# Kernel optimization log

Hardware: AMD Instinct MI355X
Metric: run time of the kernel (lower is better)

The kernel has to match this reference:

```python
import jax, jax.numpy as jnp
import numpy as np

N = 50000
E = 800000
D = 128
H = 8
DH = D // H


def setup_inputs() -> dict:
    key = jax.random.key(0)
    ks = jax.random.split(key, 8)
    x = jax.random.normal(ks[0], (N, D), dtype=jnp.float32)
    src = jax.random.randint(ks[1], (E,), 0, N, dtype=jnp.int32)
    dst = jax.random.randint(ks[2], (E,), 0, N, dtype=jnp.int32)
    s = 1.0 / np.sqrt(D)
    w_qkv = jax.random.uniform(ks[3], (3 * D, D), jnp.float32, -s, s)
    b_qkv = jax.random.uniform(ks[4], (3 * D,), jnp.float32, -s, s)
    w_out = jax.random.uniform(ks[5], (D, D), jnp.float32, -s, s)
    b_out = jax.random.uniform(ks[6], (D,), jnp.float32, -s, s)
    return {"x": x, "src": src, "dst": dst, "w_qkv": w_qkv, "b_qkv": b_qkv,
            "w_out": w_out, "b_out": b_out}


def reference(x, src, dst, w_qkv, b_qkv, w_out, b_out):
    n = x.shape[0]
    coef = 1.0 / np.sqrt(DH)
    qkv = (x @ w_qkv.T + b_qkv).reshape(n, H, 3 * DH)
    q, k, v = qkv[..., :DH], qkv[..., DH:2 * DH], qkv[..., 2 * DH:]
    # per-edge scores: dot(k[src], q[dst]) per head -> [E, H]
    scores = jnp.einsum('ehd,ehd->eh', k[src], q[dst]) * coef
    # edge softmax over edges sharing the same destination node
    smax = jax.ops.segment_max(scores, dst, num_segments=n)  # [N, H]
    smax = jnp.where(jnp.isfinite(smax), smax, 0.0)
    ex = jnp.exp(scores - smax[dst])                          # [E, H]
    denom = jax.ops.segment_sum(ex, dst, num_segments=n)      # [N, H]
    probs = ex / jnp.maximum(denom[dst], 1e-30)
    # weighted aggregation of source values -> [N, H, DH]
    agg = jax.ops.segment_sum(probs[:, :, None] * v[src], dst, num_segments=n)
    out = agg.reshape(n, D) @ w_out.T + b_out
    return out
```

## Files before the change

kernel.cpp:

```cpp
#include <hip/hip_runtime.h>
#include <math.h>

#define DD   128
#define NQKV 384
#define CAP  128

typedef __attribute__((ext_vector_type(8))) short          bf16x8;
typedef __attribute__((ext_vector_type(8))) unsigned short ushort8;
typedef __attribute__((ext_vector_type(4))) float          f32x4;

__device__ __forceinline__ unsigned short f2bf(float f) {
    unsigned u = __float_as_uint(f);
    u += 0x7fffu + ((u >> 16) & 1u);
    return (unsigned short)(u >> 16);
}
__device__ __forceinline__ float bf2f(unsigned short h) {
    return __uint_as_float(((unsigned)h) << 16);
}
__device__ __forceinline__ float bflo(unsigned u) { return __uint_as_float(u << 16); }
__device__ __forceinline__ float bfhi(unsigned u) { return __uint_as_float(u & 0xffff0000u); }

#define NWQ8 (NQKV * DD / 8)
#define NWO8 (DD * DD / 8)

__global__ void prep_kernel(const float* __restrict__ w_qkv, const float* __restrict__ w_out,
                            unsigned short* __restrict__ wq_hi, unsigned short* __restrict__ wq_lo,
                            unsigned short* __restrict__ wo_hi, unsigned short* __restrict__ wo_lo,
                            int* __restrict__ counts, int nzc4) {
    int i = blockIdx.x * blockDim.x + threadIdx.x;
    if (i < nzc4) {
        ((int4*)counts)[i] = make_int4(0, 0, 0, 0);
        return;
    }
    int j = i - nzc4;
    const float* srcp;
    unsigned short *hip_, *lop_;
    if (j < NWQ8)            { srcp = w_qkv + (size_t)j * 8;          hip_ = wq_hi + (size_t)j * 8;          lop_ = wq_lo + (size_t)j * 8; }
    else if (j < NWQ8+NWO8)  { int k = j - NWQ8; srcp = w_out + (size_t)k * 8; hip_ = wo_hi + (size_t)k * 8; lop_ = wo_lo + (size_t)k * 8; }
    else return;
    const float4* p = (const float4*)srcp;
    float4 a = p[0], b = p[1];
    float v[8] = {a.x, a.y, a.z, a.w, b.x, b.y, b.z, b.w};
    ushort8 vh, vl;
    #pragma unroll
    for (int t = 0; t < 8; ++t) {
        unsigned short h = f2bf(v[t]);
        vh[t] = h;
        vl[t] = f2bf(v[t] - bf2f(h));
    }
    *(ushort8*)hip_ = vh;
    *(ushort8*)lop_ = vl;
}

__global__ void scatter_fixed_kernel(const int* __restrict__ src, const int* __restrict__ dst,
                                     int* __restrict__ counts, int* __restrict__ lists, int E) {
    int t = blockIdx.x * blockDim.x + threadIdx.x;
    int base = t * 8;
    if (base >= E) return;
    if (base + 8 <= E) {
        int4 d0 = *(const int4*)(dst + base);
        int4 d1 = *(const int4*)(dst + base + 4);
        int4 s0 = *(const int4*)(src + base);
        int4 s1 = *(const int4*)(src + base + 4);
        int dd[8] = {d0.x, d0.y, d0.z, d0.w, d1.x, d1.y, d1.z, d1.w};
        int ss[8] = {s0.x, s0.y, s0.z, s0.w, s1.x, s1.y, s1.z, s1.w};
        int pos[8];
        #pragma unroll
        for (int i = 0; i < 8; ++i) pos[i] = atomicAdd(&counts[dd[i]], 1);
        #pragma unroll
        for (int i = 0; i < 8; ++i)
            if (pos[i] < CAP) lists[(size_t)dd[i] * CAP + pos[i]] = ss[i];
    } else {
        for (int e = base; e < E; ++e) {
            int d = dst[e];
            int pos = atomicAdd(&counts[d], 1);
            if (pos < CAP) lists[(size_t)d * CAP + pos] = src[e];
        }
    }
}

#define TM 128
#define TN 128
#define LDA 40

__global__ __launch_bounds__(256, 3) void qkv_gemm_kernel(
    const float* __restrict__ X,
    const unsigned short* __restrict__ Bh, const unsigned short* __restrict__ Bl,
    const float* __restrict__ bias, unsigned short* __restrict__ Cq,
    unsigned short* __restrict__ Ck, unsigned short* __restrict__ Cv, int M)
{
    __shared__ unsigned short As[TM * LDA];
    __shared__ unsigned short Bs_h[TN * LDA];
    __shared__ unsigned short Bs_l[TN * LDA];

    const int tid  = threadIdx.x;
    const int l    = tid & 63;
    const int wv   = tid >> 6;
    const int quad = l >> 4;
    const int l15  = l & 15;
    const int wm   = (wv & 1) * 64;
    const int wn   = (wv >> 1) * 64;
    const int n0   = blockIdx.x * TN;
    const int m0   = blockIdx.y * TM;

    f32x4 acc[4][4];
    #pragma unroll
    for (int i = 0; i < 4; ++i)
        #pragma unroll
        for (int j = 0; j < 4; ++j) acc[i][j] = (f32x4)0.f;

    #pragma unroll
    for (int kc = 0; kc < DD; kc += 32) {
        #pragma unroll
        for (int it = 0; it < 2; ++it) {
            int idx = tid + it * 256;
            int row = idx >> 2;
            int pc  = idx & 3;
            int loff = row * LDA + pc * 8;
            ushort8 va = 0;
            if (m0 + row < M) {
                const float4* xp = (const float4*)(X + (size_t)(m0 + row) * DD + kc + pc * 8);
                float4 a0 = xp[0], a1 = xp[1];
                float v[8] = {a0.x,a0.y,a0.z,a0.w,a1.x,a1.y,a1.z,a1.w};
                #pragma unroll
                for (int t = 0; t < 8; ++t) va[t] = f2bf(v[t]);
            }
            *(ushort8*)&As[loff] = va;
            size_t gb = (size_t)(n0 + row) * DD + kc + pc * 8;
            *(ushort8*)&Bs_h[loff] = *(const ushort8*)(Bh + gb);
            *(ushort8*)&Bs_l[loff] = *(const ushort8*)(Bl + gb);
        }
        __syncthreads();

        bf16x8 ah[4], bh[4], bl[4];
        #pragma unroll
        for (int mt = 0; mt < 4; ++mt)
            ah[mt] = *(const bf16x8*)&As[(wm + mt * 16 + l15) * LDA + quad * 8];
        #pragma unroll
        for (int nt = 0; nt < 4; ++nt) {
            int off = (wn + nt * 16 + l15) * LDA + quad * 8;
            bh[nt] = *(const bf16x8*)&Bs_h[off];
            bl[nt] = *(const bf16x8*)&Bs_l[off];
        }
        #pragma unroll
        for (int mt = 0; mt < 4; ++mt)
            #pragma unroll
            for (int nt = 0; nt < 4; ++nt) {
                acc[mt][nt] = __builtin_amdgcn_mfma_f32_16x16x32_bf16(ah[mt], bh[nt], acc[mt][nt], 0, 0, 0);
                acc[mt][nt] = __builtin_amdgcn_mfma_f32_16x16x32_bf16(ah[mt], bl[nt], acc[mt][nt], 0, 0, 0);
            }
        __syncthreads();
    }

    #pragma unroll
    for (int nt = 0; nt < 4; ++nt) {
        int j = n0 + wn + nt * 16 + l15;
        float bj = bias[j];
        int h = j / 48;
        int r = j - h * 48;
        int seg = (r >= 32) ? 2 : ((r >= 16) ? 1 : 0);
        int bc  = h * 16 + r - seg * 16;
        unsigned short* dstp = (seg == 0 ? Cq : (seg == 1 ? Ck : Cv));
        #pragma unroll
        for (int mt = 0; mt < 4; ++mt)
            #pragma unroll
            for (int rr = 0; rr < 4; ++rr) {
                int m = m0 + wm + mt * 16 + quad * 4 + rr;
                if (m < M) dstp[(size_t)m * DD + bc] = f2bf(acc[mt][nt][rr] + bj);
            }
    }
}

__global__ __launch_bounds__(256, 3) void out_gemm_kernel(
    const unsigned short* __restrict__ A,
    const unsigned short* __restrict__ Bh, const unsigned short* __restrict__ Bl,
    const float* __restrict__ bias, float* __restrict__ C, int M)
{
    __shared__ unsigned short As[TM * LDA];
    __shared__ unsigned short Bs_h[TN * LDA];
    __shared__ unsigned short Bs_l[TN * LDA];

    const int tid  = threadIdx.x;
    const int l    = tid & 63;
    const int wv   = tid >> 6;
    const int quad = l >> 4;
    const int l15  = l & 15;
    const int wm   = (wv & 1) * 64;
    const int wn   = (wv >> 1) * 64;
    const int m0   = blockIdx.x * TM;

    f32x4 acc[4][4];
    #pragma unroll
    for (int i = 0; i < 4; ++i)
        #pragma unroll
        for (int j = 0; j < 4; ++j) acc[i][j] = (f32x4)0.f;

    #pragma unroll
    for (int kc = 0; kc < DD; kc += 32) {
        #pragma unroll
        for (int it = 0; it < 2; ++it) {
            int idx = tid + it * 256;
            int row = idx >> 2;
            int pc  = idx & 3;
            int loff = row * LDA + pc * 8;
            ushort8 va = 0;
            if (m0 + row < M)
                va = *(const ushort8*)(A + (size_t)(m0 + row) * DD + kc + pc * 8);
            *(ushort8*)&As[loff] = va;
            size_t gb = (size_t)row * DD + kc + pc * 8;
            *(ushort8*)&Bs_h[loff] = *(const ushort8*)(Bh + gb);
            *(ushort8*)&Bs_l[loff] = *(const ushort8*)(Bl + gb);
        }
        __syncthreads();

        bf16x8 ah[4], bh[4], bl[4];
        #pragma unroll
        for (int mt = 0; mt < 4; ++mt)
            ah[mt] = *(const bf16x8*)&As[(wm + mt * 16 + l15) * LDA + quad * 8];
        #pragma unroll
        for (int nt = 0; nt < 4; ++nt) {
            int off = (wn + nt * 16 + l15) * LDA + quad * 8;
            bh[nt] = *(const bf16x8*)&Bs_h[off];
            bl[nt] = *(const bf16x8*)&Bs_l[off];
        }
        #pragma unroll
        for (int mt = 0; mt < 4; ++mt)
            #pragma unroll
            for (int nt = 0; nt < 4; ++nt) {
                acc[mt][nt] = __builtin_amdgcn_mfma_f32_16x16x32_bf16(ah[mt], bh[nt], acc[mt][nt], 0, 0, 0);
                acc[mt][nt] = __builtin_amdgcn_mfma_f32_16x16x32_bf16(ah[mt], bl[nt], acc[mt][nt], 0, 0, 0);
            }
        __syncthreads();
    }

    #pragma unroll
    for (int nt = 0; nt < 4; ++nt) {
        int j = wn + nt * 16 + l15;
        float bj = bias[j];
        #pragma unroll
        for (int mt = 0; mt < 4; ++mt)
            #pragma unroll
            for (int rr = 0; rr < 4; ++rr) {
                int m = m0 + wm + mt * 16 + quad * 4 + rr;
                if (m < M) C[(size_t)m * DD + j] = acc[mt][nt][rr] + bj;
            }
    }
}

__global__ __launch_bounds__(256) void wave_attn_kernel(
    const unsigned short* __restrict__ qbf, const unsigned short* __restrict__ kbf,
    const unsigned short* __restrict__ vbf, const int* __restrict__ lists,
    const int* __restrict__ counts,
    unsigned short* __restrict__ agg, int N)
{
    const int lane = threadIdx.x & 63;
    const int n = blockIdx.x * 4 + (threadIdx.x >> 6);
    if (n >= N) return;

    const int h = lane >> 3;
    const int e = lane & 7;

    const int deg = min(counts[n], CAP);
    const size_t obase = (size_t)n * DD + 2 * lane;
    if (deg == 0) {
        *(unsigned*)(agg + obase) = 0u;
        return;
    }

    const int row0 = n * CAP;

    const uint4* qp = (const uint4*)(qbf + (size_t)n * DD + h * 16);
    const uint4 qa = qp[0], qb = qp[1];
    const float4 q0 = make_float4(bflo(qa.x), bfhi(qa.x), bflo(qa.y), bfhi(qa.y));
    const float4 q1 = make_float4(bflo(qa.z), bfhi(qa.z), bflo(qa.w), bfhi(qa.w));
    const float4 q2 = make_float4(bflo(qb.x), bfhi(qb.x), bflo(qb.y), bfhi(qb.y));
    const float4 q3 = make_float4(bflo(qb.z), bfhi(qb.z), bflo(qb.w), bfhi(qb.w));

    int cur = lists[row0 + min(e, deg - 1)];
    int nxt = lists[row0 + min(8 + e, deg - 1)];

    const uint4* kp0 = (const uint4*)(kbf + (size_t)cur * DD + h * 16);
    uint4 ka = kp0[0], kb = kp0[1];
    unsigned vv[8];
    #pragma unroll
    for (int ee = 0; ee < 8; ++ee)
        vv[ee] = *(const unsigned*)(vbf + (size_t)__shfl(cur, ee) * DD + 2 * lane);

    float l_run = 0.f;
    float acc0 = 0.f, acc1 = 0.f;

    for (int c = 0; c < deg; c += 8) {
        const int cnt = min(8, deg - c);
        const bool more = (c + 8 < deg);

        const int nn = lists[row0 + min(c + 16 + e, deg - 1)];

        uint4 k1a = ka, k1b = kb;
        unsigned vn[8];
        #pragma unroll
        for (int ee = 0; ee < 8; ++ee) vn[ee] = vv[ee];
        if (more) {
            const uint4* kp = (const uint4*)(kbf + (size_t)nxt * DD + h * 16);
            k1a = kp[0]; k1b = kp[1];
            #pragma unroll
            for (int ee = 0; ee < 8; ++ee)
                vn[ee] = *(const unsigned*)(vbf + (size_t)__shfl(nxt, ee) * DD + 2 * lane);
        }

        float s = bflo(ka.x)*q0.x + bfhi(ka.x)*q0.y + bflo(ka.y)*q0.z + bfhi(ka.y)*q0.w
                + bflo(ka.z)*q1.x + bfhi(ka.z)*q1.y + bflo(ka.w)*q1.z + bfhi(ka.w)*q1.w
                + bflo(kb.x)*q2.x + bfhi(kb.x)*q2.y + bflo(kb.y)*q2.z + bfhi(kb.y)*q2.w
                + bflo(kb.z)*q3.x + bfhi(kb.z)*q3.y + bflo(kb.w)*q3.z + bfhi(kb.w)*q3.w;

        const float p = (e < cnt) ? __expf(s * 0.25f) : 0.f;
        l_run += p;

        #pragma unroll
        for (int ee = 0; ee < 8; ++ee) {
            const float pe = __shfl(p, (lane & 0x38) | ee);
            acc0 = fmaf(pe, bflo(vv[ee]), acc0);
            acc1 = fmaf(pe, bfhi(vv[ee]), acc1);
        }

        ka = k1a; kb = k1b;
        #pragma unroll
        for (int ee = 0; ee < 8; ++ee) vv[ee] = vn[ee];
        cur = nxt; nxt = nn;
    }

    l_run += __shfl_xor(l_run, 1);
    l_run += __shfl_xor(l_run, 2);
    l_run += __shfl_xor(l_run, 4);

    const float inv = 1.f / fmaxf(l_run, 1e-30f);
    const float o0 = acc0 * inv, o1 = acc1 * inv;
    *(unsigned*)(agg + obase) = (unsigned)f2bf(o0) | ((unsigned)f2bf(o1) << 16);
}

extern "C" void kernel_launch(void* const* d_in, const int* in_sizes, int n_in,
                              void* d_out, int out_size, void* d_ws, size_t ws_size,
                              hipStream_t stream) {
    const float* x     = (const float*)d_in[0];
    const int*   src   = (const int*)  d_in[1];
    const int*   dst   = (const int*)  d_in[2];
    const float* w_qkv = (const float*)d_in[3];
    const float* b_qkv = (const float*)d_in[4];
    const float* w_out = (const float*)d_in[5];
    const float* b_out = (const float*)d_in[6];
    float* out = (float*)d_out;

    const int N = in_sizes[0] / DD;
    const int E = in_sizes[1];

    typedef unsigned short u16;
    char* ws = (char*)d_ws;
    u16* qbf   = (u16*)ws;   ws += (size_t)N * DD * sizeof(u16);
    u16* kbf   = (u16*)ws;   ws += (size_t)N * DD * sizeof(u16);
    u16* vbf   = (u16*)ws;   ws += (size_t)N * DD * sizeof(u16);
    u16* aggb  = (u16*)ws;   ws += (size_t)N * DD * sizeof(u16);
    u16* wq_hi = (u16*)ws;   ws += (size_t)NQKV * DD * sizeof(u16);
    u16* wq_lo = (u16*)ws;   ws += (size_t)NQKV * DD * sizeof(u16);
    u16* wo_hi = (u16*)ws;   ws += (size_t)DD * DD * sizeof(u16);
    u16* wo_lo = (u16*)ws;   ws += (size_t)DD * DD * sizeof(u16);
    int* counts = (int*)ws;  ws += (size_t)((N + 3) / 4 * 4) * sizeof(int);
    int* lists  = (int*)ws;  ws += (size_t)N * CAP * sizeof(int);

    const int nzc4 = (N + 3) / 4;
    const int npb  = (nzc4 + NWQ8 + NWO8 + 255) / 256;
    const int nsb  = ((E + 7) / 8 + 255) / 256;
    const int MB   = (N + TM - 1) / TM;

    prep_kernel<<<npb, 256, 0, stream>>>(w_qkv, w_out, wq_hi, wq_lo, wo_hi, wo_lo,
                                         counts, nzc4);
    scatter_fixed_kernel<<<nsb, 256, 0, stream>>>(src, dst, counts, lists, E);

    qkv_gemm_kernel<<<dim3(NQKV / TN, MB), 256, 0, stream>>>(
        x, wq_hi, wq_lo, b_qkv, qbf, kbf, vbf, N);

    wave_attn_kernel<<<(N + 3) / 4, 256, 0, stream>>>(
        qbf, kbf, vbf, lists, counts, aggb, N);

    out_gemm_kernel<<<MB, 256, 0, stream>>>(
        aggb, wo_hi, wo_lo, b_out, out, N);
}
```

Baseline: 235.4 us.

## Stage full-K A tile once in LDS and read weights directly from global

```diff
diff --git a/kernel.cpp b/kernel.cpp
--- a/kernel.cpp
+++ b/kernel.cpp
@@ -81,17 +81,15 @@
 
 #define TM 128
 #define TN 128
-#define LDA 40
-
-__global__ __launch_bounds__(256, 3) void qkv_gemm_kernel(
+#define LDK 136
+
+__global__ __launch_bounds__(256, 2) void qkv_gemm_kernel(
     const float* __restrict__ X,
     const unsigned short* __restrict__ Bh, const unsigned short* __restrict__ Bl,
     const float* __restrict__ bias, unsigned short* __restrict__ Cq,
     unsigned short* __restrict__ Ck, unsigned short* __restrict__ Cv, int M)
 {
-    __shared__ unsigned short As[TM * LDA];
-    __shared__ unsigned short Bs_h[TN * LDA];
-    __shared__ unsigned short Bs_l[TN * LDA];
+    __shared__ unsigned short As[TM * LDK];
 
     const int tid  = threadIdx.x;
     const int l    = tid & 63;
@@ -100,8 +98,25 @@
     const int l15  = l & 15;
     const int wm   = (wv & 1) * 64;
     const int wn   = (wv >> 1) * 64;
-    const int n0   = blockIdx.x * TN;
-    const int m0   = blockIdx.y * TM;
+    const int m0   = blockIdx.x * TM;
+    const int n0   = blockIdx.y * TN;
+
+    #pragma unroll
+    for (int it = 0; it < 8; ++it) {
+        int idx = tid + it * 256;
+        int row = idx >> 4;
+        int pc  = idx & 15;
+        ushort8 va = 0;
+        if (m0 + row < M) {
+            const float4* xp = (const float4*)(X + (size_t)(m0 + row) * DD + pc * 8);
+            float4 a0 = xp[0], a1 = xp[1];
+            float v[8] = {a0.x,a0.y,a0.z,a0.w,a1.x,a1.y,a1.z,a1.w};
+            #pragma unroll
+            for (int t = 0; t < 8; ++t) va[t] = f2bf(v[t]);
+        }
+        *(ushort8*)&As[row * LDK + pc * 8] = va;
+    }
+    __syncthreads();
 
     f32x4 acc[4][4];
     #pragma unroll
@@ -110,38 +125,18 @@
         for (int j = 0; j < 4; ++j) acc[i][j] = (f32x4)0.f;
 
     #pragma unroll
-    for (int kc = 0; kc < DD; kc += 32) {
-        #pragma unroll
-        for (int it = 0; it < 2; ++it) {
-            int idx = tid + it * 256;
-            int row = idx >> 2;
-            int pc  = idx & 3;
-            int loff = row * LDA + pc * 8;
-            ushort8 va = 0;
-            if (m0 + row < M) {
-                const float4* xp = (const float4*)(X + (size_t)(m0 + row) * DD + kc + pc * 8);
-                float4 a0 = xp[0], a1 = xp[1];
-                float v[8] = {a0.x,a0.y,a0.z,a0.w,a1.x,a1.y,a1.z,a1.w};
-                #pragma unroll
-                for (int t = 0; t < 8; ++t) va[t] = f2bf(v[t]);
-            }
-            *(ushort8*)&As[loff] = va;
-            size_t gb = (size_t)(n0 + row) * DD + kc + pc * 8;
-            *(ushort8*)&Bs_h[loff] = *(const ushort8*)(Bh + gb);
-            *(ushort8*)&Bs_l[loff] = *(const ushort8*)(Bl + gb);
-        }
-        __syncthreads();
-
+    for (int kk = 0; kk < 4; ++kk) {
+        const int ko = kk * 32 + quad * 8;
         bf16x8 ah[4], bh[4], bl[4];
         #pragma unroll
-        for (int mt = 0; mt < 4; ++mt)
-            ah[mt] = *(const bf16x8*)&As[(wm + mt * 16 + l15) * LDA + quad * 8];
-        #pragma unroll
         for (int nt = 0; nt < 4; ++nt) {
-            int off = (wn + nt * 16 + l15) * LDA + quad * 8;
-            bh[nt] = *(const bf16x8*)&Bs_h[off];
-            bl[nt] = *(const bf16x8*)&Bs_l[off];
-        }
+            size_t gb = (size_t)(n0 + wn + nt * 16 + l15) * DD + ko;
+            bh[nt] = *(const bf16x8*)(Bh + gb);
+            bl[nt] = *(const bf16x8*)(Bl + gb);
+        }
+        #pragma unroll
+        for (int mt = 0; mt < 4; ++mt)
+            ah[mt] = *(const bf16x8*)&As[(wm + mt * 16 + l15) * LDK + ko];
         #pragma unroll
         for (int mt = 0; mt < 4; ++mt)
             #pragma unroll
@@ -149,7 +144,6 @@
                 acc[mt][nt] = __builtin_amdgcn_mfma_f32_16x16x32_bf16(ah[mt], bh[nt], acc[mt][nt], 0, 0, 0);
                 acc[mt][nt] = __builtin_amdgcn_mfma_f32_16x16x32_bf16(ah[mt], bl[nt], acc[mt][nt], 0, 0, 0);
             }
-        __syncthreads();
     }
 
     #pragma unroll
@@ -171,14 +165,12 @@
     }
 }
 
-__global__ __launch_bounds__(256, 3) void out_gemm_kernel(
+__global__ __launch_bounds__(256, 2) void out_gemm_kernel(
     const unsigned short* __restrict__ A,
     const unsigned short* __restrict__ Bh, const unsigned short* __restrict__ Bl,
     const float* __restrict__ bias, float* __restrict__ C, int M)
 {
-    __shared__ unsigned short As[TM * LDA];
-    __shared__ unsigned short Bs_h[TN * LDA];
-    __shared__ unsigned short Bs_l[TN * LDA];
+    __shared__ unsigned short As[TM * LDK];
 
     const int tid  = threadIdx.x;
     const int l    = tid & 63;
@@ -189,6 +181,18 @@
     const int wn   = (wv >> 1) * 64;
     const int m0   = blockIdx.x * TM;
 
+    #pragma unroll
+    for (int it = 0; it < 8; ++it) {
+        int idx = tid + it * 256;
+        int row = idx >> 4;
+        int pc  = idx & 15;
+        ushort8 va = 0;
+        if (m0 + row < M)
+            va = *(const ushort8*)(A + (size_t)(m0 + row) * DD + pc * 8);
+        *(ushort8*)&As[row * LDK + pc * 8] = va;
+    }
+    __syncthreads();
+
     f32x4 acc[4][4];
     #pragma unroll
     for (int i = 0; i < 4; ++i)
@@ -196,33 +200,18 @@
         for (int j = 0; j < 4; ++j) acc[i][j] = (f32x4)0.f;
 
     #pragma unroll
-    for (int kc = 0; kc < DD; kc += 32) {
-        #pragma unroll
-        for (int it = 0; it < 2; ++it) {
-            int idx = tid + it * 256;
-            int row = idx >> 2;
-            int pc  = idx & 3;
-            int loff = row * LDA + pc * 8;
-            ushort8 va = 0;
-            if (m0 + row < M)
-                va = *(const ushort8*)(A + (size_t)(m0 + row) * DD + kc + pc * 8);
-            *(ushort8*)&As[loff] = va;
-            size_t gb = (size_t)row * DD + kc + pc * 8;
-            *(ushort8*)&Bs_h[loff] = *(const ushort8*)(Bh + gb);
-            *(ushort8*)&Bs_l[loff] = *(const ushort8*)(Bl + gb);
-        }
-        __syncthreads();
-
+    for (int kk = 0; kk < 4; ++kk) {
+        const int ko = kk * 32 + quad * 8;
         bf16x8 ah[4], bh[4], bl[4];
         #pragma unroll
-        for (int mt = 0; mt < 4; ++mt)
-            ah[mt] = *(const bf16x8*)&As[(wm + mt * 16 + l15) * LDA + quad * 8];
-        #pragma unroll
         for (int nt = 0; nt < 4; ++nt) {
-            int off = (wn + nt * 16 + l15) * LDA + quad * 8;
-            bh[nt] = *(const bf16x8*)&Bs_h[off];
-            bl[nt] = *(const bf16x8*)&Bs_l[off];
-        }
+            size_t gb = (size_t)(wn + nt * 16 + l15) * DD + ko;
+            bh[nt] = *(const bf16x8*)(Bh + gb);
+            bl[nt] = *(const bf16x8*)(Bl + gb);
+        }
+        #pragma unroll
+        for (int mt = 0; mt < 4; ++mt)
+            ah[mt] = *(const bf16x8*)&As[(wm + mt * 16 + l15) * LDK + ko];
         #pragma unroll
         for (int mt = 0; mt < 4; ++mt)
             #pragma unroll
@@ -230,7 +219,6 @@
                 acc[mt][nt] = __builtin_amdgcn_mfma_f32_16x16x32_bf16(ah[mt], bh[nt], acc[mt][nt], 0, 0, 0);
                 acc[mt][nt] = __builtin_amdgcn_mfma_f32_16x16x32_bf16(ah[mt], bl[nt], acc[mt][nt], 0, 0, 0);
             }
-        __syncthreads();
     }
 
     #pragma unroll
@@ -374,7 +362,7 @@
                                          counts, nzc4);
     scatter_fixed_kernel<<<nsb, 256, 0, stream>>>(src, dst, counts, lists, E);
 
-    qkv_gemm_kernel<<<dim3(NQKV / TN, MB), 256, 0, stream>>>(
+    qkv_gemm_kernel<<<dim3(MB, NQKV / TN), 256, 0, stream>>>(
         x, wq_hi, wq_lo, b_qkv, qbf, kbf, vbf, N);
 
     wave_attn_kernel<<<(N + 3) / 4, 256, 0, stream>>>(
```

Result: slower. 252.1 us (+7.1%).

## Fuse weight bf16 split into GEMMs, memset counts, packed-float attention math

Applied to the files above, without the earlier changes.

```diff
diff --git a/kernel.cpp b/kernel.cpp
--- a/kernel.cpp
+++ b/kernel.cpp
@@ -8,6 +8,7 @@
 typedef __attribute__((ext_vector_type(8))) short          bf16x8;
 typedef __attribute__((ext_vector_type(8))) unsigned short ushort8;
 typedef __attribute__((ext_vector_type(4))) float          f32x4;
+typedef __attribute__((ext_vector_type(2))) float          f32x2;
 
 __device__ __forceinline__ unsigned short f2bf(float f) {
     unsigned u = __float_as_uint(f);
@@ -19,37 +20,8 @@
 }
 __device__ __forceinline__ float bflo(unsigned u) { return __uint_as_float(u << 16); }
 __device__ __forceinline__ float bfhi(unsigned u) { return __uint_as_float(u & 0xffff0000u); }
-
-#define NWQ8 (NQKV * DD / 8)
-#define NWO8 (DD * DD / 8)
-
-__global__ void prep_kernel(const float* __restrict__ w_qkv, const float* __restrict__ w_out,
-                            unsigned short* __restrict__ wq_hi, unsigned short* __restrict__ wq_lo,
-                            unsigned short* __restrict__ wo_hi, unsigned short* __restrict__ wo_lo,
-                            int* __restrict__ counts, int nzc4) {
-    int i = blockIdx.x * blockDim.x + threadIdx.x;
-    if (i < nzc4) {
-        ((int4*)counts)[i] = make_int4(0, 0, 0, 0);
-        return;
-    }
-    int j = i - nzc4;
-    const float* srcp;
-    unsigned short *hip_, *lop_;
-    if (j < NWQ8)            { srcp = w_qkv + (size_t)j * 8;          hip_ = wq_hi + (size_t)j * 8;          lop_ = wq_lo + (size_t)j * 8; }
-    else if (j < NWQ8+NWO8)  { int k = j - NWQ8; srcp = w_out + (size_t)k * 8; hip_ = wo_hi + (size_t)k * 8; lop_ = wo_lo + (size_t)k * 8; }
-    else return;
-    const float4* p = (const float4*)srcp;
-    float4 a = p[0], b = p[1];
-    float v[8] = {a.x, a.y, a.z, a.w, b.x, b.y, b.z, b.w};
-    ushort8 vh, vl;
-    #pragma unroll
-    for (int t = 0; t < 8; ++t) {
-        unsigned short h = f2bf(v[t]);
-        vh[t] = h;
-        vl[t] = f2bf(v[t] - bf2f(h));
-    }
-    *(ushort8*)hip_ = vh;
-    *(ushort8*)lop_ = vl;
+__device__ __forceinline__ f32x2 unpk(unsigned u) {
+    f32x2 r; r.x = bflo(u); r.y = bfhi(u); return r;
 }
 
 __global__ void scatter_fixed_kernel(const int* __restrict__ src, const int* __restrict__ dst,
@@ -84,8 +56,7 @@
 #define LDA 40
 
 __global__ __launch_bounds__(256, 3) void qkv_gemm_kernel(
-    const float* __restrict__ X,
-    const unsigned short* __restrict__ Bh, const unsigned short* __restrict__ Bl,
+    const float* __restrict__ X, const float* __restrict__ W,
     const float* __restrict__ bias, unsigned short* __restrict__ Cq,
     unsigned short* __restrict__ Ck, unsigned short* __restrict__ Cv, int M)
 {
@@ -126,9 +97,18 @@
                 for (int t = 0; t < 8; ++t) va[t] = f2bf(v[t]);
             }
             *(ushort8*)&As[loff] = va;
-            size_t gb = (size_t)(n0 + row) * DD + kc + pc * 8;
-            *(ushort8*)&Bs_h[loff] = *(const ushort8*)(Bh + gb);
-            *(ushort8*)&Bs_l[loff] = *(const ushort8*)(Bl + gb);
+            const float4* wp = (const float4*)(W + (size_t)(n0 + row) * DD + kc + pc * 8);
+            float4 b0 = wp[0], b1 = wp[1];
+            float wvv[8] = {b0.x,b0.y,b0.z,b0.w,b1.x,b1.y,b1.z,b1.w};
+            ushort8 vh, vl;
+            #pragma unroll
+            for (int t = 0; t < 8; ++t) {
+                unsigned short hh = f2bf(wvv[t]);
+                vh[t] = hh;
+                vl[t] = f2bf(wvv[t] - bf2f(hh));
+            }
+            *(ushort8*)&Bs_h[loff] = vh;
+            *(ushort8*)&Bs_l[loff] = vl;
         }
         __syncthreads();
 
@@ -172,8 +152,7 @@
 }
 
 __global__ __launch_bounds__(256, 3) void out_gemm_kernel(
-    const unsigned short* __restrict__ A,
-    const unsigned short* __restrict__ Bh, const unsigned short* __restrict__ Bl,
+    const unsigned short* __restrict__ A, const float* __restrict__ W,
     const float* __restrict__ bias, float* __restrict__ C, int M)
 {
     __shared__ unsigned short As[TM * LDA];
@@ -207,9 +186,18 @@
             if (m0 + row < M)
                 va = *(const ushort8*)(A + (size_t)(m0 + row) * DD + kc + pc * 8);
             *(ushort8*)&As[loff] = va;
-            size_t gb = (size_t)row * DD + kc + pc * 8;
-            *(ushort8*)&Bs_h[loff] = *(const ushort8*)(Bh + gb);
-            *(ushort8*)&Bs_l[loff] = *(const ushort8*)(Bl + gb);
+            const float4* wp = (const float4*)(W + (size_t)row * DD + kc + pc * 8);
+            float4 b0 = wp[0], b1 = wp[1];
+            float wvv[8] = {b0.x,b0.y,b0.z,b0.w,b1.x,b1.y,b1.z,b1.w};
+            ushort8 vh, vl;
+            #pragma unroll
+            for (int t = 0; t < 8; ++t) {
+                unsigned short hh = f2bf(wvv[t]);
+                vh[t] = hh;
+                vl[t] = f2bf(wvv[t] - bf2f(hh));
+            }
+            *(ushort8*)&Bs_h[loff] = vh;
+            *(ushort8*)&Bs_l[loff] = vl;
         }
         __syncthreads();
 
@@ -271,10 +259,8 @@
 
     const uint4* qp = (const uint4*)(qbf + (size_t)n * DD + h * 16);
     const uint4 qa = qp[0], qb = qp[1];
-    const float4 q0 = make_float4(bflo(qa.x), bfhi(qa.x), bflo(qa.y), bfhi(qa.y));
-    const float4 q1 = make_float4(bflo(qa.z), bfhi(qa.z), bflo(qa.w), bfhi(qa.w));
-    const float4 q2 = make_float4(bflo(qb.x), bfhi(qb.x), bflo(qb.y), bfhi(qb.y));
-    const float4 q3 = make_float4(bflo(qb.z), bfhi(qb.z), bflo(qb.w), bfhi(qb.w));
+    const f32x2 qv[8] = { unpk(qa.x), unpk(qa.y), unpk(qa.z), unpk(qa.w),
+                          unpk(qb.x), unpk(qb.y), unpk(qb.z), unpk(qb.w) };
 
     int cur = lists[row0 + min(e, deg - 1)];
     int nxt = lists[row0 + min(8 + e, deg - 1)];
@@ -287,7 +273,7 @@
         vv[ee] = *(const unsigned*)(vbf + (size_t)__shfl(cur, ee) * DD + 2 * lane);
 
     float l_run = 0.f;
-    float acc0 = 0.f, acc1 = 0.f;
+    f32x2 acc2 = (f32x2)0.f;
 
     for (int c = 0; c < deg; c += 8) {
         const int cnt = min(8, deg - c);
@@ -307,10 +293,15 @@
                 vn[ee] = *(const unsigned*)(vbf + (size_t)__shfl(nxt, ee) * DD + 2 * lane);
         }
 
-        float s = bflo(ka.x)*q0.x + bfhi(ka.x)*q0.y + bflo(ka.y)*q0.z + bfhi(ka.y)*q0.w
-                + bflo(ka.z)*q1.x + bfhi(ka.z)*q1.y + bflo(ka.w)*q1.z + bfhi(ka.w)*q1.w
-                + bflo(kb.x)*q2.x + bfhi(kb.x)*q2.y + bflo(kb.y)*q2.z + bfhi(kb.y)*q2.w
-                + bflo(kb.z)*q3.x + bfhi(kb.z)*q3.y + bflo(kb.w)*q3.z + bfhi(kb.w)*q3.w;
+        f32x2 d = unpk(ka.x) * qv[0];
+        d = unpk(ka.y) * qv[1] + d;
+        d = unpk(ka.z) * qv[2] + d;
+        d = unpk(ka.w) * qv[3] + d;
+        d = unpk(kb.x) * qv[4] + d;
+        d = unpk(kb.y) * qv[5] + d;
+        d = unpk(kb.z) * qv[6] + d;
+        d = unpk(kb.w) * qv[7] + d;
+        const float s = d.x + d.y;
 
         const float p = (e < cnt) ? __expf(s * 0.25f) : 0.f;
         l_run += p;
@@ -318,8 +309,7 @@
         #pragma unroll
         for (int ee = 0; ee < 8; ++ee) {
             const float pe = __shfl(p, (lane & 0x38) | ee);
-            acc0 = fmaf(pe, bflo(vv[ee]), acc0);
-            acc1 = fmaf(pe, bfhi(vv[ee]), acc1);
+            acc2 = unpk(vv[ee]) * pe + acc2;
         }
 
         ka = k1a; kb = k1b;
@@ -333,7 +323,7 @@
     l_run += __shfl_xor(l_run, 4);
 
     const float inv = 1.f / fmaxf(l_run, 1e-30f);
-    const float o0 = acc0 * inv, o1 = acc1 * inv;
+    const float o0 = acc2.x * inv, o1 = acc2.y * inv;
     *(unsigned*)(agg + obase) = (unsigned)f2bf(o0) | ((unsigned)f2bf(o1) << 16);
 }
 
@@ -358,28 +348,22 @@
     u16* kbf   = (u16*)ws;   ws += (size_t)N * DD * sizeof(u16);
     u16* vbf   = (u16*)ws;   ws += (size_t)N * DD * sizeof(u16);
     u16* aggb  = (u16*)ws;   ws += (size_t)N * DD * sizeof(u16);
-    u16* wq_hi = (u16*)ws;   ws += (size_t)NQKV * DD * sizeof(u16);
-    u16* wq_lo = (u16*)ws;   ws += (size_t)NQKV * DD * sizeof(u16);
-    u16* wo_hi = (u16*)ws;   ws += (size_t)DD * DD * sizeof(u16);
-    u16* wo_lo = (u16*)ws;   ws += (size_t)DD * DD * sizeof(u16);
-    int* counts = (int*)ws;  ws += (size_t)((N + 3) / 4 * 4) * sizeof(int);
+    int* counts = (int*)ws;  ws += (size_t)N * sizeof(int);
     int* lists  = (int*)ws;  ws += (size_t)N * CAP * sizeof(int);
 
-    const int nzc4 = (N + 3) / 4;
-    const int npb  = (nzc4 + NWQ8 + NWO8 + 255) / 256;
-    const int nsb  = ((E + 7) / 8 + 255) / 256;
-    const int MB   = (N + TM - 1) / TM;
-
-    prep_kernel<<<npb, 256, 0, stream>>>(w_qkv, w_out, wq_hi, wq_lo, wo_hi, wo_lo,
-                                         counts, nzc4);
+    const int nsb = ((E + 7) / 8 + 255) / 256;
+    const int MB  = (N + TM - 1) / TM;
+
+    hipMemsetAsync(counts, 0, (size_t)N * sizeof(int), stream);
+
     scatter_fixed_kernel<<<nsb, 256, 0, stream>>>(src, dst, counts, lists, E);
 
     qkv_gemm_kernel<<<dim3(NQKV / TN, MB), 256, 0, stream>>>(
-        x, wq_hi, wq_lo, b_qkv, qbf, kbf, vbf, N);
+        x, w_qkv, b_qkv, qbf, kbf, vbf, N);
 
     wave_attn_kernel<<<(N + 3) / 4, 256, 0, stream>>>(
         qbf, kbf, vbf, lists, counts, aggb, N);
 
     out_gemm_kernel<<<MB, 256, 0, stream>>>(
-        aggb, wo_hi, wo_lo, b_out, out, N);
-}
+        aggb, w_out, b_out, out, N);
+}
```

New measurement: 240.5 us. 2.2% more time.
